# Optimization experiments

Measured on AMD Instinct MI355X. Metric: run time of the kernel, lower is better.

## Reference

```python
import jax, jax.numpy as jnp
import numpy as np

V, E, H, D, DFF, NB, C, B, T = 32000, 512, 256, 512, 2048, 4, 16, 32, 512
PAD, BOS, EOS = 0, 1, 2


def positional_encoding(t, d):
    pos = jnp.arange(t, dtype=jnp.float32)[:, None]
    i = jnp.arange(0, d, 2, dtype=jnp.float32)
    div = jnp.exp(-(jnp.log(10000.0)) * i / d)
    pe = jnp.zeros((t, d), jnp.float32)
    pe = pe.at[:, 0::2].set(jnp.sin(pos * div))
    pe = pe.at[:, 1::2].set(jnp.cos(pos * div))
    return pe


def layernorm(x, g, b, eps=1e-5):
    mu = jnp.mean(x, -1, keepdims=True)
    var = jnp.mean((x - mu) ** 2, -1, keepdims=True)
    return (x - mu) * jax.lax.rsqrt(var + eps) * g + b


def gru_dir(xs, w_ih, w_hh, b_ih, b_hh, reverse):
    # xs: (B,T,E); precompute input projections for all t (one big GEMM)
    gi = jnp.einsum('bte,ge->btg', xs, w_ih) + b_ih  # (B,T,3H)
    h0 = jnp.zeros((xs.shape[0], H), xs.dtype)

    def step(h, gi_t):
        gh = h @ w_hh.T + b_hh
        i_r, i_z, i_n = jnp.split(gi_t, 3, -1)
        h_r, h_z, h_n = jnp.split(gh, 3, -1)
        r = jax.nn.sigmoid(i_r + h_r)
        z = jax.nn.sigmoid(i_z + h_z)
        n = jnp.tanh(i_n + r * h_n)
        h_new = (1.0 - z) * n + z * h
        return h_new, h_new

    _, hs = jax.lax.scan(step, h0, jnp.swapaxes(gi, 0, 1), reverse=reverse)
    return jnp.swapaxes(hs, 0, 1)  # (B,T,H)


def forward(x, y, embed_W, w_ih_f, w_hh_f, b_ih_f, b_hh_f, w_ih_b, w_hh_b, b_ih_b, b_hh_b,
            ff_w1, ff_b1, ff_w2, ff_b2, ln_g, ln_b, fc_w, fc_b, trans):
    h = embed_W[x]                                   # (B,T,E)
    h = h + positional_encoding(h.shape[1], E)[None]
    hf = gru_dir(h, w_ih_f, w_hh_f, b_ih_f, b_hh_f, False)
    hb = gru_dir(h, w_ih_b, w_hh_b, b_ih_b, b_hh_b, True)
    h = jnp.concatenate([hf, hb], -1)                # (B,T,D)
    for i in range(NB):                              # FeedForward blocks (residual + LN)
        ff = jax.nn.relu(h @ ff_w1[i] + ff_b1[i]) @ ff_w2[i] + ff_b2[i]
        h = layernorm(h + ff, ln_g[i], ln_b[i])
    logits = h @ fc_w + fc_b                         # (B,T,C) emissions

    # --- CRF viterbi decode ---
    mask = (y != PAD)                                # (B,T) bool
    emit = jnp.swapaxes(logits, 0, 1)                # (T,B,C)
    m = jnp.swapaxes(mask, 0, 1)                     # (T,B)
    score0 = trans[BOS][None] + emit[0]              # (B,C)

    def vstep(score, inp):
        e_t, m_t = inp                               # (B,C), (B,)
        cand = score[:, :, None] + trans[None] + e_t[:, None, :]  # (B,prev,cur)
        new = jnp.max(cand, axis=1)
        bp = jnp.argmax(cand, axis=1)                # (B,C)
        new = jnp.where(m_t[:, None], new, score)
        return new, bp

    final, bps = jax.lax.scan(vstep, score0, (emit[1:], m[1:]))  # bps: (T-1,B,C)
    final = final + trans[:, EOS][None]
    best_score = jnp.max(final, -1)                  # (B,)
    last_tag = jnp.argmax(final, -1)                 # (B,)

    def back(tag, inp):
        bp_t, m_t = inp
        prev = jnp.take_along_axis(bp_t, tag[:, None], axis=1)[:, 0]
        prev = jnp.where(m_t, prev, tag)
        return prev, tag

    first_tag, rest = jax.lax.scan(back, last_tag, (bps, m[1:]), reverse=True)
    path = jnp.swapaxes(jnp.concatenate([first_tag[None], rest], 0), 0, 1)  # (B,T)
    return best_score, path


def setup_inputs():
    key = jax.random.key(0)
    ks = jax.random.split(key, 16)
    nrm = lambda k, sh, sc: jax.random.normal(k, sh, jnp.float32) * sc
    s = 1.0 / float(np.sqrt(H))
    inp = {}
    inp['x'] = jax.random.randint(ks[0], (B, T), 1, V)
    inp['y'] = jax.random.randint(ks[1], (B, T), 0, 13) + 3  # in [3,16): no pad/bos/eos
    inp['embed_W'] = nrm(ks[2], (V, E), 0.02)
    inp['w_ih_f'] = nrm(ks[3], (3 * H, E), s); inp['w_hh_f'] = nrm(ks[4], (3 * H, H), s)
    inp['b_ih_f'] = nrm(ks[5], (3 * H,), s); inp['b_hh_f'] = nrm(ks[6], (3 * H,), s)
    inp['w_ih_b'] = nrm(ks[7], (3 * H, E), s); inp['w_hh_b'] = nrm(ks[8], (3 * H, H), s)
    inp['b_ih_b'] = nrm(ks[9], (3 * H,), s); inp['b_hh_b'] = nrm(ks[10], (3 * H,), s)
    inp['ff_w1'] = nrm(ks[11], (NB, D, DFF), 1.0 / float(np.sqrt(D)))
    inp['ff_b1'] = jnp.zeros((NB, DFF), jnp.float32)
    inp['ff_w2'] = nrm(ks[12], (NB, DFF, D), 1.0 / float(np.sqrt(DFF)))
    inp['ff_b2'] = jnp.zeros((NB, D), jnp.float32)
    inp['ln_g'] = jnp.ones((NB, D), jnp.float32); inp['ln_b'] = jnp.zeros((NB, D), jnp.float32)
    inp['fc_w'] = nrm(ks[13], (D, C), 1.0 / float(np.sqrt(D)))
    inp['fc_b'] = jnp.zeros((C,), jnp.float32)
    inp['trans'] = nrm(ks[14], (C, C), 0.1)
    return inp


def reference(x, y, embed_W, w_ih_f, w_hh_f, b_ih_f, b_hh_f, w_ih_b, w_hh_b, b_ih_b, b_hh_b,
              ff_w1, ff_b1, ff_w2, ff_b2, ln_g, ln_b, fc_w, fc_b, trans):
    return forward(x, y, embed_W, w_ih_f, w_hh_f, b_ih_f, b_hh_f, w_ih_b, w_hh_b, b_ih_b, b_hh_b,
                   ff_w1, ff_b1, ff_w2, ff_b2, ln_g, ln_b, fc_w, fc_b, trans)
```

## Files before the change

### kernel.cpp

```cpp
#include <hip/hip_runtime.h>

#define DEV __device__ __forceinline__

using short8 = __attribute__((ext_vector_type(8))) short;
using f32x4  = __attribute__((ext_vector_type(4))) float;

DEV float b2f(short s) {
  union { unsigned u; float f; } c;
  c.u = ((unsigned)(unsigned short)s) << 16;
  return c.f;
}
DEV short f2b(float f) {
  union { float f; unsigned u; } c; c.f = f;
  unsigned u = c.u + 0x7fffu + ((c.u >> 16) & 1u);
  return (short)(u >> 16);
}
DEV float fast_sigmoid(float x) {
  return __builtin_amdgcn_rcpf(1.f + __expf(-x));
}
DEV float fast_tanh(float x) {
  return 1.f - 2.f * __builtin_amdgcn_rcpf(1.f + __expf(2.f * x));
}
DEV void async_ld16(const void* g, void* lds) {
  __builtin_amdgcn_global_load_lds(
      (const __attribute__((address_space(1))) void*)(unsigned long long)g,
      (__attribute__((address_space(3))) void*)(unsigned)(unsigned long long)lds,
      16, 0, 0);
}

__global__ __launch_bounds__(256) void k_cvt2(const float* __restrict__ a, const float* __restrict__ b,
                                              short* __restrict__ oa, short* __restrict__ ob) {
  int blk = blockIdx.x;
  const float* in; short* out; int base;
  if (blk < 384) { in = a; out = oa; base = blk; }
  else           { in = b; out = ob; base = blk - 384; }
  int i = base * 256 + threadIdx.x;
  f32x4 v = *(const f32x4*)(in + (size_t)i * 4);
  short4 o;
#pragma unroll
  for (int j = 0; j < 4; j++) ((short*)&o)[j] = f2b(v[j]);
  *(short4*)(out + (size_t)i * 4) = o;
}

__global__ __launch_bounds__(256) void k_w8(const float* __restrict__ wf,
                                            const float* __restrict__ wb,
                                            long* __restrict__ out) {
  int flat = blockIdx.x * 256 + threadIdx.x;
  int lane = flat & 63;
  int r1 = flat >> 6;
  int kb = r1 & 7;
  int r2 = r1 >> 3;
  int g = r2 % 3;
  int r3 = r2 / 3;
  int v = r3 & 15;
  int d = r3 >> 4;
  const float* w = d ? wb : wf;
  int row = g * 256 + v * 16 + (lane & 15);
  int k0 = kb * 32 + (lane >> 4) * 8;
  const float* p = w + (size_t)row * 256 + k0;
  f32x4 f0 = *(const f32x4*)(p);
  f32x4 f1 = *(const f32x4*)(p + 4);
  int u0 = __builtin_amdgcn_cvt_pk_fp8_f32(f0[0], f0[1], 0, false);
  u0 = __builtin_amdgcn_cvt_pk_fp8_f32(f0[2], f0[3], u0, true);
  int u1 = __builtin_amdgcn_cvt_pk_fp8_f32(f1[0], f1[1], 0, false);
  u1 = __builtin_amdgcn_cvt_pk_fp8_f32(f1[2], f1[3], u1, true);
  out[flat] = ((long)(unsigned)u1 << 32) | (unsigned)u0;
}

__global__ __launch_bounds__(256) void k_embed(const int* __restrict__ x,
                                               const float* __restrict__ W,
                                               short* __restrict__ h0) {
  int flat = blockIdx.x * 256 + threadIdx.x;
  int row  = flat >> 6;
  int e0   = (flat & 63) << 3;
  int tok  = x[row];
  int t    = row & 511;
  const float* wp = W + (size_t)tok * 512 + e0;
  float v[8];
  *(f32x4*)v       = *(const f32x4*)(wp);
  *(f32x4*)(v + 4) = *(const f32x4*)(wp + 4);
  short8 o;
#pragma unroll
  for (int i = 0; i < 8; i += 2) {
    float f = expf(-9.210340371976184f * (float)(e0 + i) * (1.f / 512.f));
    float ang = (float)t * f;
    o[i]     = f2b(v[i]     + sinf(ang));
    o[i + 1] = f2b(v[i + 1] + cosf(ang));
  }
  *(short8*)(h0 + (size_t)flat * 8) = o;
}

__global__ __launch_bounds__(256) void k_transcvt(const float* __restrict__ in0,
                                                  short* __restrict__ out0, int R, int C) {
  __shared__ float tile[32][33];
  int mat = blockIdx.x >> 10;
  const float* in = in0 + (size_t)mat * 1048576;
  short* out = out0 + (size_t)mat * 1048576;
  int blk = blockIdx.x & 1023;
  int ct = C >> 5;
  int bc = blk % ct, br = blk / ct;
  int r0 = br << 5, c0 = bc << 5;
  for (int i = threadIdx.x; i < 1024; i += 256) {
    int r = i >> 5, c = i & 31;
    tile[r][c] = in[(size_t)(r0 + r) * C + c0 + c];
  }
  __syncthreads();
  for (int i = threadIdx.x; i < 1024; i += 256) {
    int c = i >> 5, r = i & 31;
    out[(size_t)(c0 + c) * R + r0 + r] = f2b(tile[r][c]);
  }
}

template <int MODE>
__global__ __launch_bounds__(256) void k_gemm(const short* __restrict__ A,
    const short* __restrict__ B, const float* __restrict__ bias,
    float* __restrict__ Cf, short* __restrict__ Cb, int M, int N, int K) {
  __shared__ short smA[8192];
  __shared__ short smB[8192];
  const int tid = threadIdx.x, lane = tid & 63, wave = tid >> 6;
  const int m15 = lane & 15, q8 = (lane >> 4) << 3;
  const int tn = N >> 7;
  const int bm = blockIdx.x / tn, bn = blockIdx.x % tn;
  const int wm = wave & 1, wn = wave >> 1;
  const f32x4 z4 = {0.f, 0.f, 0.f, 0.f};
  f32x4 acc[4][4];
#pragma unroll
  for (int i = 0; i < 4; i++)
#pragma unroll
    for (int j = 0; j < 4; j++) acc[i][j] = z4;

  for (int k0 = 0; k0 < K; k0 += 64) {
#pragma unroll
    for (int is = 0; is < 4; is++) {
      int c = is * 4 + wave;
      int mb = c & 7, kb = c >> 3;
      async_ld16(A + (size_t)(bm * 128 + mb * 16 + m15) * K + k0 + kb * 32 + q8, smA + c * 512);
      async_ld16(B + (size_t)(bn * 128 + mb * 16 + m15) * K + k0 + kb * 32 + q8, smB + c * 512);
    }
    __syncthreads();
#pragma unroll
    for (int kk = 0; kk < 2; kk++) {
      short8 af[4], bf[4];
#pragma unroll
      for (int i = 0; i < 4; i++)
        af[i] = *(const short8*)(smA + (kk * 8 + wm * 4 + i) * 512 + lane * 8);
#pragma unroll
      for (int j = 0; j < 4; j++)
        bf[j] = *(const short8*)(smB + (kk * 8 + wn * 4 + j) * 512 + lane * 8);
#pragma unroll
      for (int i = 0; i < 4; i++)
#pragma unroll
        for (int j = 0; j < 4; j++)
          acc[i][j] = __builtin_amdgcn_mfma_f32_16x16x32_bf16(af[i], bf[j], acc[i][j], 0, 0, 0);
    }
    __syncthreads();
  }
#pragma unroll
  for (int j = 0; j < 4; j++) {
    int col = bn * 128 + wn * 64 + j * 16 + m15;
    float bv = bias[col];
#pragma unroll
    for (int i = 0; i < 4; i++) {
      int row0 = bm * 128 + wm * 64 + i * 16 + ((lane >> 4) << 2);
#pragma unroll
      for (int r = 0; r < 4; r++) {
        float v = acc[i][j][r] + bv;
        int rr = row0 + r;
        if (MODE == 0) {
          Cf[(size_t)rr * N + col] = v;
        } else if (MODE == 1) {
          if (v < 0.f) v = 0.f;
          Cb[(size_t)rr * N + col] = f2b(v);
        } else {
          Cb[((size_t)((rr & 511) * 32 + (rr >> 9))) * 768 + col] = f2b(v);
        }
      }
    }
  }
}

__global__ __launch_bounds__(1024) void k_gru(
    const long* __restrict__ w8,
    const float* __restrict__ bhh_f, const float* __restrict__ bhh_b,
    const short* __restrict__ gi16_f, const short* __restrict__ gi16_b,
    short* __restrict__ hcat16) {
  __shared__ char  hb[2][4352];
  __shared__ float smG[3][4][256];
  const int blk = blockIdx.x;
  const int d = blk & 1, bg = blk >> 1;
  const int tid = threadIdx.x, lane = tid & 63, v = tid >> 6;
  const int m15 = lane & 15, quad = lane >> 4, q8 = quad * 8;
  const int brow = tid >> 8, bcol = tid & 255;
  const float* bhh = d ? bhh_b : bhh_f;
  const short* gi  = d ? gi16_b : gi16_f;

  long Bf[3][8];
  {
    const long* wp = w8 + (size_t)(d * 16 + v) * 1536;
#pragma unroll
    for (int g = 0; g < 3; g++)
#pragma unroll
      for (int kb = 0; kb < 8; kb++)
        Bf[g][kb] = wp[(g * 8 + kb) * 64 + lane];
  }
  float bh[3];
#pragma unroll
  for (int g = 0; g < 3; g++) bh[g] = bhh[g * 256 + bcol];

  for (int i = tid; i < 2176; i += 1024) ((int*)hb)[i] = 0;

  const int t0 = d ? 511 : 0;
  const int tstep = d ? -1 : 1;
  const long gdelta = (long)tstep * 32 * 768;
  const short* gp0 = gi + ((size_t)t0 * 32 + bg * 4 + brow) * 768 + bcol;
  const short* gp1 = gp0 + 256;
  const short* gp2 = gp0 + 512;
  short* hout = hcat16 + ((size_t)t0 * 32 + bg * 4 + brow) * 512 + d * 256 + bcol;
  const long hdelta = (long)tstep * 32 * 512;

  float gic0 = b2f(*gp0), gic1 = b2f(*gp1), gic2 = b2f(*gp2);
  gp0 += gdelta; gp1 += gdelta; gp2 += gdelta;
  float hprev = 0.f;
  const f32x4 z4 = {0.f, 0.f, 0.f, 0.f};
  __syncthreads();

  for (int s = 0; s < 512; s++) {
    short n0 = 0, n1 = 0, n2 = 0;
    if (s < 511) {
      n0 = *gp0; n1 = *gp1; n2 = *gp2;
      gp0 += gdelta; gp1 += gdelta; gp2 += gdelta;
    }
    const char* hs = hb[s & 1];
    f32x4 acc0 = z4, acc1 = z4, acc2 = z4;
#pragma unroll
    for (int kb = 0; kb < 8; kb++) {
      long a = *(const long*)(hs + m15 * 272 + kb * 32 + q8);
      acc0 = __builtin_amdgcn_mfma_f32_16x16x32_fp8_fp8(a, Bf[0][kb], acc0, 0, 0, 0);
      acc1 = __builtin_amdgcn_mfma_f32_16x16x32_fp8_fp8(a, Bf[1][kb], acc1, 0, 0, 0);
      acc2 = __builtin_amdgcn_mfma_f32_16x16x32_fp8_fp8(a, Bf[2][kb], acc2, 0, 0, 0);
    }
    if (quad == 0) {
      int c = v * 16 + m15;
#pragma unroll
      for (int i = 0; i < 4; i++) {
        smG[0][i][c] = acc0[i];
        smG[1][i][c] = acc1[i];
        smG[2][i][c] = acc2[i];
      }
    }
    __syncthreads();
    float gr = smG[0][brow][bcol];
    float gz = smG[1][brow][bcol];
    float gn = smG[2][brow][bcol];
    float r = fast_sigmoid(gic0 + gr + bh[0]);
    float z = fast_sigmoid(gic1 + gz + bh[1]);
    float n = fast_tanh(gic2 + r * (gn + bh[2]));
    float h = (1.f - z) * n + z * hprev;
    hprev = h;
    int p8 = __builtin_amdgcn_cvt_pk_fp8_f32(h, h, 0, false);
    hb[(s + 1) & 1][brow * 272 + bcol] = (char)(p8 & 0xff);
    *hout = f2b(h);
    hout += hdelta;
    gic0 = b2f(n0); gic1 = b2f(n1); gic2 = b2f(n2);
    __syncthreads();
  }
}

template <int FIRST>
__global__ __launch_bounds__(256) void k_ln(const float* __restrict__ hinf,
    const float* __restrict__ ff, const float* __restrict__ gw,
    const float* __restrict__ bw, float* __restrict__ hout, short* __restrict__ h16) {
  int row = blockIdx.x * 4 + (threadIdx.x >> 6);
  int lane = threadIdx.x & 63;
  size_t base = (size_t)row * 512 + lane * 8;
  f32x4 x0, x1;
  if (FIRST) {
    short8 hv = *(const short8*)(h16 + base);
#pragma unroll
    for (int i = 0; i < 4; i++) { x0[i] = b2f(hv[i]); x1[i] = b2f(hv[4 + i]); }
  } else {
    x0 = *(const f32x4*)(hinf + base);
    x1 = *(const f32x4*)(hinf + base + 4);
  }
  f32x4 y0 = *(const f32x4*)(ff + base);
  f32x4 y1 = *(const f32x4*)(ff + base + 4);
  x0 += y0; x1 += y1;
  float s = x0[0] + x0[1] + x0[2] + x0[3] + x1[0] + x1[1] + x1[2] + x1[3];
#pragma unroll
  for (int off = 32; off >= 1; off >>= 1) s += __shfl_xor(s, off);
  float mu = s * (1.f / 512.f);
  float vv = 0.f;
#pragma unroll
  for (int i = 0; i < 4; i++) { float d0 = x0[i] - mu, d1 = x1[i] - mu; vv += d0 * d0 + d1 * d1; }
#pragma unroll
  for (int off = 32; off >= 1; off >>= 1) vv += __shfl_xor(vv, off);
  float rs = rsqrtf(vv * (1.f / 512.f) + 1e-5f);
  int e = lane * 8;
  f32x4 g0 = *(const f32x4*)(gw + e), g1 = *(const f32x4*)(gw + e + 4);
  f32x4 bb0 = *(const f32x4*)(bw + e), bb1 = *(const f32x4*)(bw + e + 4);
  f32x4 o0, o1; short8 ob;
#pragma unroll
  for (int i = 0; i < 4; i++) {
    float a = (x0[i] - mu) * rs * g0[i] + bb0[i];
    float b = (x1[i] - mu) * rs * g1[i] + bb1[i];
    o0[i] = a; o1[i] = b; ob[i] = f2b(a); ob[4 + i] = f2b(b);
  }
  *(f32x4*)(hout + base) = o0;
  *(f32x4*)(hout + base + 4) = o1;
  *(short8*)(h16 + base) = ob;
}

__global__ __launch_bounds__(256) void k_fc(const float* __restrict__ h,
    const float* __restrict__ fcw, const float* __restrict__ bias,
    float* __restrict__ logits) {
  int row = blockIdx.x * 4 + (threadIdx.x >> 6);
  int lane = threadIdx.x & 63;
  int c = lane & 15, part = lane >> 4;
  const float* ph = h + (size_t)row * 512 + part * 128;
  const float* pw = fcw + (size_t)part * 128 * 16 + c;
  float acc = 0.f;
#pragma unroll 8
  for (int k = 0; k < 128; k += 4) {
    f32x4 hv = *(const f32x4*)(ph + k);
    acc += hv[0] * pw[(k) * 16] + hv[1] * pw[(k + 1) * 16]
         + hv[2] * pw[(k + 2) * 16] + hv[3] * pw[(k + 3) * 16];
  }
  acc += __shfl_xor(acc, 16);
  acc += __shfl_xor(acc, 32);
  if (part == 0) logits[(size_t)row * 16 + c] = acc + bias[c];
}

__global__ __launch_bounds__(64) void k_crf(const float* __restrict__ logits,
    const int* __restrict__ y, const float* __restrict__ trans,
    float* __restrict__ out) {
  __shared__ float tr[16][16];
  __shared__ unsigned char bp[511][16];
  int b = blockIdx.x, lane = threadIdx.x;
  for (int i = lane; i < 256; i += 64) tr[i >> 4][i & 15] = trans[i];
  __syncthreads();
  int cur = lane & 15;
  const float* lg = logits + (size_t)b * 16;
  const int* yb = y + b * 512;
  float score = tr[1][cur] + lg[cur];
  float e_next = lg[512 + cur];
  int y_next = yb[1];
  for (int t = 1; t < 512; t++) {
    float e = e_next; int ym = y_next;
    if (t < 511) { e_next = lg[(t + 1) * 512 + cur]; y_next = yb[t + 1]; }
    float best = -3.4e38f; int arg = 0;
#pragma unroll
    for (int p = 0; p < 16; p++) {
      float cand = __shfl(score, p) + tr[p][cur];
      if (cand > best) { best = cand; arg = p; }
    }
    if (lane < 16) bp[t - 1][cur] = (unsigned char)arg;
    float ns = best + e;
    if (ym == 0) ns = score;
    score = ns;
  }
  score += tr[cur][2];
  float best = -3.4e38f; int argb = 0;
#pragma unroll
  for (int p = 0; p < 16; p++) {
    float sp = __shfl(score, p);
    if (sp > best) { best = sp; argb = p; }
  }
  __syncthreads();
  if (lane == 0) {
    out[b] = best;
    float* po = out + 32 + (size_t)b * 512;
    int tag = argb;
    po[511] = (float)tag;
    for (int t = 511; t >= 1; t--) {
      int prev = bp[t - 1][tag];
      if (yb[t] == 0) prev = tag;
      po[t - 1] = (float)prev;
      tag = prev;
    }
  }
}

extern "C" void kernel_launch(void* const* d_in, const int* in_sizes, int n_in,
                              void* d_out, int out_size, void* d_ws, size_t ws_size,
                              hipStream_t stream) {
  const int*   x      = (const int*)d_in[0];
  const int*   y      = (const int*)d_in[1];
  const float* embedW = (const float*)d_in[2];
  const float* w_ih_f = (const float*)d_in[3];
  const float* w_hh_f = (const float*)d_in[4];
  const float* b_ih_f = (const float*)d_in[5];
  const float* b_hh_f = (const float*)d_in[6];
  const float* w_ih_b = (const float*)d_in[7];
  const float* w_hh_b = (const float*)d_in[8];
  const float* b_ih_b = (const float*)d_in[9];
  const float* b_hh_b = (const float*)d_in[10];
  const float* ff_w1  = (const float*)d_in[11];
  const float* ff_b1  = (const float*)d_in[12];
  const float* ff_w2  = (const float*)d_in[13];
  const float* ff_b2  = (const float*)d_in[14];
  const float* ln_g   = (const float*)d_in[15];
  const float* ln_b   = (const float*)d_in[16];
  const float* fc_w   = (const float*)d_in[17];
  const float* fc_b   = (const float*)d_in[18];
  const float* trans  = (const float*)d_in[19];
  float* out = (float*)d_out;

  char* ws = (char*)d_ws;
  short* h0     = (short*)(ws + 0);
  short* gi16_f = (short*)(ws + 16777216);
  short* gi16_b = (short*)(ws + 41943040);
  short* mid    = (short*)(ws + 16777216);
  float* ffout  = (float*)(ws + 83886080);
  short* wihf16 = (short*)(ws + 117440512);
  short* wihb16 = (short*)(ws + 118226944);
  long*  w8     = (long*) (ws + 119013376);
  short* w1t    = (short*)(ws + 119799808);
  short* w2t    = (short*)(ws + 128188416);
  short* hcat16 = (short*)(ws + 136577024);
  float* hres   = (float*)(ws + 153354240);
  float* logits = (float*)(ws + 186908672);

  k_embed<<<4096, 256, 0, stream>>>(x, embedW, h0);
  k_cvt2<<<768, 256, 0, stream>>>(w_ih_f, w_ih_b, wihf16, wihb16);
  k_w8<<<192, 256, 0, stream>>>(w_hh_f, w_hh_b, w8);
  k_transcvt<<<4096, 256, 0, stream>>>(ff_w1, w1t, 512, 2048);
  k_transcvt<<<4096, 256, 0, stream>>>(ff_w2, w2t, 2048, 512);

  k_gemm<2><<<768, 256, 0, stream>>>(h0, wihf16, b_ih_f, nullptr, gi16_f, 16384, 768, 512);
  k_gemm<2><<<768, 256, 0, stream>>>(h0, wihb16, b_ih_b, nullptr, gi16_b, 16384, 768, 512);

  k_gru<<<16, 1024, 0, stream>>>(w8, b_hh_f, b_hh_b, gi16_f, gi16_b, hcat16);

  for (int i = 0; i < 4; i++) {
    k_gemm<1><<<2048, 256, 0, stream>>>(hcat16, w1t + (size_t)i * 1048576, ff_b1 + i * 2048,
                                        nullptr, mid, 16384, 2048, 512);
    k_gemm<0><<<512, 256, 0, stream>>>(mid, w2t + (size_t)i * 1048576, ff_b2 + i * 512,
                                       ffout, nullptr, 16384, 512, 2048);
    if (i == 0)
      k_ln<1><<<4096, 256, 0, stream>>>(nullptr, ffout, ln_g, ln_b, hres, hcat16);
    else
      k_ln<0><<<4096, 256, 0, stream>>>(hres, ffout, ln_g + i * 512, ln_b + i * 512, hres, hcat16);
  }
  k_fc<<<4096, 256, 0, stream>>>(hres, fc_w, fc_b, logits);
  k_crf<<<32, 64, 0, stream>>>(logits, y, trans, out);
}
```

Before: 1.832 ms.

## Remap GRU gate math to MFMA owner wave, drop mid-step barrier, batch h stores

Each wave now handles the gate nonlinearity for the 16 columns it computed with MFMA, reading the accumulators back through a per-wave LDS slice. This removes one of the two block-wide barriers per timestep. The bf16 hidden-state writes to global are buffered in registers and flushed every 8 steps to take them off the recurrence path. The per-wave LDS handoff relies on in-wave ordering with no explicit wave barrier, and the flush still issues scalar 2-byte stores.

```diff
diff --git a/kernel.cpp b/kernel.cpp
--- a/kernel.cpp
+++ b/kernel.cpp
@@ -185,12 +185,13 @@
     const short* __restrict__ gi16_f, const short* __restrict__ gi16_b,
     short* __restrict__ hcat16) {
   __shared__ char  hb[2][4352];
-  __shared__ float smG[3][4][256];
+  __shared__ float smG[16][200];
   const int blk = blockIdx.x;
   const int d = blk & 1, bg = blk >> 1;
   const int tid = threadIdx.x, lane = tid & 63, v = tid >> 6;
   const int m15 = lane & 15, quad = lane >> 4, q8 = quad * 8;
-  const int brow = tid >> 8, bcol = tid & 255;
+  const int col = v * 16 + m15;
+  const int brow = quad;
   const float* bhh = d ? bhh_b : bhh_f;
   const short* gi  = d ? gi16_b : gi16_f;
 
@@ -205,22 +206,22 @@
   }
   float bh[3];
 #pragma unroll
-  for (int g = 0; g < 3; g++) bh[g] = bhh[g * 256 + bcol];
+  for (int g = 0; g < 3; g++) bh[g] = bhh[g * 256 + col];
 
   for (int i = tid; i < 2176; i += 1024) ((int*)hb)[i] = 0;
 
   const int t0 = d ? 511 : 0;
-  const int tstep = d ? -1 : 1;
-  const long gdelta = (long)tstep * 32 * 768;
-  const short* gp0 = gi + ((size_t)t0 * 32 + bg * 4 + brow) * 768 + bcol;
+  const long gdelta = (long)(d ? -1 : 1) * 32 * 768;
+  const long hdelta = (long)(d ? -1 : 1) * 32 * 512;
+  const short* gp0 = gi + ((size_t)t0 * 32 + bg * 4 + brow) * 768 + col;
   const short* gp1 = gp0 + 256;
   const short* gp2 = gp0 + 512;
-  short* hout = hcat16 + ((size_t)t0 * 32 + bg * 4 + brow) * 512 + d * 256 + bcol;
-  const long hdelta = (long)tstep * 32 * 512;
+  short* hflush = hcat16 + ((size_t)t0 * 32 + bg * 4 + brow) * 512 + d * 256 + col;
 
   float gic0 = b2f(*gp0), gic1 = b2f(*gp1), gic2 = b2f(*gp2);
   gp0 += gdelta; gp1 += gdelta; gp2 += gdelta;
   float hprev = 0.f;
+  unsigned obuf[4] = {0u, 0u, 0u, 0u};
   const f32x4 z4 = {0.f, 0.f, 0.f, 0.f};
   __syncthreads();
 
@@ -240,27 +241,36 @@
       acc2 = __builtin_amdgcn_mfma_f32_16x16x32_fp8_fp8(a, Bf[2][kb], acc2, 0, 0, 0);
     }
     if (quad == 0) {
-      int c = v * 16 + m15;
 #pragma unroll
       for (int i = 0; i < 4; i++) {
-        smG[0][i][c] = acc0[i];
-        smG[1][i][c] = acc1[i];
-        smG[2][i][c] = acc2[i];
+        smG[v][i * 16 + m15]       = acc0[i];
+        smG[v][64 + i * 16 + m15]  = acc1[i];
+        smG[v][128 + i * 16 + m15] = acc2[i];
       }
     }
-    __syncthreads();
-    float gr = smG[0][brow][bcol];
-    float gz = smG[1][brow][bcol];
-    float gn = smG[2][brow][bcol];
+    float gr = smG[v][lane];
+    float gz = smG[v][64 + lane];
+    float gn = smG[v][128 + lane];
     float r = fast_sigmoid(gic0 + gr + bh[0]);
     float z = fast_sigmoid(gic1 + gz + bh[1]);
     float n = fast_tanh(gic2 + r * (gn + bh[2]));
     float h = (1.f - z) * n + z * hprev;
     hprev = h;
     int p8 = __builtin_amdgcn_cvt_pk_fp8_f32(h, h, 0, false);
-    hb[(s + 1) & 1][brow * 272 + bcol] = (char)(p8 & 0xff);
-    *hout = f2b(h);
-    hout += hdelta;
+    hb[(s + 1) & 1][brow * 272 + col] = (char)(p8 & 0xff);
+    unsigned hb16 = (unsigned)(unsigned short)f2b(h);
+    int idx = s & 7;
+    if ((idx & 1) == 0) obuf[idx >> 1] = hb16;
+    else                obuf[idx >> 1] |= hb16 << 16;
+    if (idx == 7) {
+      short* p = hflush;
+#pragma unroll
+      for (int k = 0; k < 8; k++) {
+        *p = (short)(obuf[k >> 1] >> ((k & 1) * 16));
+        p += hdelta;
+      }
+      hflush += 8 * hdelta;
+    }
     gic0 = b2f(n0); gic1 = b2f(n1); gic2 = b2f(n2);
     __syncthreads();
   }
```

New measurement: 1.779 ms. 1.03x faster.
